# Kernel tuning notes

Hardware: AMD Instinct MI355X
Metric: run time of the kernel (lower is better)

The kernel has to match this reference:

```python
import jax, jax.numpy as jnp
import numpy as np

B, T, D, H = 2, 2048, 768, 12
DH = D // H  # 64

def setup_inputs() -> dict:
    key = jax.random.key(0)
    k1, k2, k3 = jax.random.split(key, 3)
    x = jax.random.normal(k1, (B, T, D), dtype=jnp.float32)
    W_qkv = jax.random.normal(k2, (D, 3 * D), dtype=jnp.float32) * (D ** -0.5)
    b_qkv = jax.random.normal(k3, (3 * D,), dtype=jnp.float32) * 0.02
    return {"x": x, "W_qkv": W_qkv, "b_qkv": b_qkv}

def reference(x, W_qkv, b_qkv):
    b, t, d = x.shape
    qkv = x @ W_qkv + b_qkv  # [b, t, 3*d]
    # 'b t (qkv h d) -> qkv b h t d'
    qkv = qkv.reshape(b, t, 3, H, DH).transpose(2, 0, 3, 1, 4)
    q, k, v = qkv[0], qkv[1], qkv[2]  # each [b, h, t, dh]
    scale = DH ** -0.5
    scores = jnp.einsum('bhid,bhjd->bhij', q, k) * scale  # [b, h, t, t]
    attn = jax.nn.softmax(scores, axis=-1)
    out = jnp.einsum('bhij,bhjd->bhid', attn, v)  # [b, h, t, dh]
    # 'b h t d -> b t (h d)'
    return out.transpose(0, 2, 1, 3).reshape(b, t, d)
```

## Files before the change

### kernel.cpp

```cpp
#include <hip/hip_runtime.h>
#include <hip/hip_bf16.h>
#include <stdint.h>

typedef __bf16 bf16_t;
typedef __bf16 v8bf  __attribute__((ext_vector_type(8)));
typedef __bf16 v4bf  __attribute__((ext_vector_type(4)));
typedef float  f32x4 __attribute__((ext_vector_type(4)));
typedef unsigned short u16x8 __attribute__((ext_vector_type(8)));

#define B_   2
#define T_   2048
#define D_   768
#define H_   12
#define DH_  64
#define N3_  2304
#define M_   4096
#define SPLIT_ 2

__device__ __forceinline__ void gll16(const void* g, void* l) {
  __builtin_amdgcn_global_load_lds(
      (const __attribute__((address_space(1))) void*)g,
      (__attribute__((address_space(3))) void*)l,
      16, 0, 0);
}

__device__ __forceinline__ float bf2f(unsigned short u) {
  union { unsigned u; float f; } x; x.u = ((unsigned)u) << 16; return x.f;
}

__global__ __launch_bounds__(256) void k_conv_x(const float* __restrict__ x,
                                                bf16_t* __restrict__ xb, int n4) {
  int i = blockIdx.x * 256 + threadIdx.x;
  if (i < n4) {
    float4 v = ((const float4*)x)[i];
    v4bf o = {(bf16_t)v.x, (bf16_t)v.y, (bf16_t)v.z, (bf16_t)v.w};
    *(v4bf*)(xb + (size_t)i * 4) = o;
  }
}

__global__ __launch_bounds__(256) void k_conv_wt(const float* __restrict__ W,
                                                 bf16_t* __restrict__ Wt) {
  __shared__ bf16_t tile[64 * 64];
  const int tid = threadIdx.x;
  const int n0 = blockIdx.x * 64;
  const int k0 = blockIdx.y * 64;
  #pragma unroll
  for (int rr = 0; rr < 4; ++rr) {
    int k  = rr * 16 + (tid >> 4);
    int gr = tid & 15;
    float4 v = *(const float4*)(W + (size_t)(k0 + k) * N3_ + n0 + gr * 4);
    v4bf o = {(bf16_t)v.x, (bf16_t)v.y, (bf16_t)v.z, (bf16_t)v.w};
    *(v4bf*)(tile + k * 64 + ((gr ^ (k & 15)) << 2)) = o;
  }
  __syncthreads();
  const int n = tid & 63, q = tid >> 6;
  bf16_t outv[16] __attribute__((aligned(16)));
  #pragma unroll
  for (int tt = 0; tt < 16; ++tt) {
    int k = q * 16 + tt;
    outv[tt] = tile[k * 64 + (((n >> 2) ^ (k & 15)) << 2) + (n & 3)];
  }
  bf16_t* dst = Wt + (size_t)(n0 + n) * D_ + k0 + q * 16;
  *(u16x8*)dst       = *(const u16x8*)outv;
  *((u16x8*)dst + 1) = *(const u16x8*)(outv + 8);
}

#define BK 32
__global__ __launch_bounds__(256) void k_gemm(const bf16_t* __restrict__ A,
                                              const bf16_t* __restrict__ Bt,
                                              const float*  __restrict__ bias,
                                              bf16_t* __restrict__ Cq,
                                              bf16_t* __restrict__ vt) {
  __shared__ bf16_t As[128 * BK];
  __shared__ bf16_t Bs[128 * BK];
  const int tid  = threadIdx.x;
  const int wave = tid >> 6, lane = tid & 63;
  const int g = lane >> 4, c = lane & 15;
  const int wy = wave >> 1, wx = wave & 1;
  const int bm = blockIdx.y * 128, bn = blockIdx.x * 128;

  const f32x4 zf = {0.f, 0.f, 0.f, 0.f};
  f32x4 acc[4][4];
  #pragma unroll
  for (int i = 0; i < 4; ++i)
    #pragma unroll
    for (int j = 0; j < 4; ++j) acc[i][j] = zf;

  const int rA = tid >> 2;
  const int kc = (tid & 3) * 8;

  for (int k0 = 0; k0 < D_; k0 += BK) {
    __syncthreads();
    #pragma unroll
    for (int cc = 0; cc < 2; ++cc) {
      gll16(A  + (size_t)(bm + cc * 64 + rA) * D_ + k0 + kc,
            (char*)As + cc * 4096 + wave * 1024);
      gll16(Bt + (size_t)(bn + cc * 64 + rA) * D_ + k0 + kc,
            (char*)Bs + cc * 4096 + wave * 1024);
    }
    __syncthreads();
    v8bf af[4], bfr[4];
    #pragma unroll
    for (int mi = 0; mi < 4; ++mi)
      af[mi] = *(const v8bf*)(As + (wy * 64 + mi * 16 + c) * BK + g * 8);
    #pragma unroll
    for (int ni = 0; ni < 4; ++ni)
      bfr[ni] = *(const v8bf*)(Bs + (wx * 64 + ni * 16 + c) * BK + g * 8);
    #pragma unroll
    for (int mi = 0; mi < 4; ++mi)
      #pragma unroll
      for (int ni = 0; ni < 4; ++ni)
        acc[mi][ni] = __builtin_amdgcn_mfma_f32_16x16x32_bf16(af[mi], bfr[ni], acc[mi][ni], 0, 0, 0);
  }

  if (bn >= 2 * D_) {
    const int hb = ((bn - 2 * D_) >> 6) + wx;
    #pragma unroll
    for (int ni = 0; ni < 4; ++ni) {
      float bv = bias[bn + wx * 64 + ni * 16 + c];
      const int d = ni * 16 + c;
      #pragma unroll
      for (int mi = 0; mi < 4; ++mi) {
        int row = bm + wy * 64 + mi * 16 + g * 4;
        int b = row >> 11, t = row & (T_ - 1);
        int tl = t & 63;
        int sp = (t & ~63) | (tl & 35) | ((tl & 12) << 1) | ((tl & 16) >> 2);
        v4bf o = {(bf16_t)(acc[mi][ni][0] + bv), (bf16_t)(acc[mi][ni][1] + bv),
                  (bf16_t)(acc[mi][ni][2] + bv), (bf16_t)(acc[mi][ni][3] + bv)};
        *(v4bf*)(vt + ((size_t)((b * H_ + hb) * DH_ + d)) * T_ + sp) = o;
      }
    }
  } else {
    const float qscale = (bn < D_) ? 0.18033688011112042f : 1.0f;
    #pragma unroll
    for (int ni = 0; ni < 4; ++ni) {
      float bv = bias[bn + wx * 64 + ni * 16 + c];
      #pragma unroll
      for (int mi = 0; mi < 4; ++mi) {
        int row = bm + wy * 64 + mi * 16 + g * 4;
        bf16_t* d0 = Cq + (size_t)row * N3_ + bn + wx * 64 + ni * 16 + c;
        #pragma unroll
        for (int j = 0; j < 4; ++j)
          d0[(size_t)j * N3_] = (bf16_t)((acc[mi][ni][j] + bv) * qscale);
      }
    }
  }
}

template<int SPLIT>
__global__ __launch_bounds__(256) void k_attn(const bf16_t* __restrict__ qkv,
                                              const bf16_t* __restrict__ vt,
                                              float* __restrict__ outp,
                                              float* __restrict__ lpart) {
  __shared__ __align__(16) bf16_t Ks[2][64 * 64];
  __shared__ __align__(16) bf16_t Vs[2][64 * 64];
  const int tid  = threadIdx.x;
  const int wave = tid >> 6, lane = tid & 63;
  const int g = lane >> 4, c = lane & 15;
  const int qt = blockIdx.x;
  const int bh = blockIdx.y;
  const int z  = (SPLIT > 1) ? blockIdx.z : 0;
  const int b = bh / H_, h = bh - b * H_;
  const int r0 = z * (T_ / SPLIT);

  v8bf aq[2];
  {
    const bf16_t* qb = qkv + ((size_t)(b * T_ + qt * 64 + wave * 16 + c)) * N3_ + h * DH_ + g * 8;
    aq[0] = *(const v8bf*)qb;
    aq[1] = *(const v8bf*)(qb + 32);
  }
  float lsum = 0.f;
  const f32x4 zf = {0.f, 0.f, 0.f, 0.f};
  f32x4 oacc[4];
  #pragma unroll
  for (int ni = 0; ni < 4; ++ni) oacc[ni] = zf;

  const int rS  = tid >> 3;
  const int grS = tid & 7;
  const bf16_t* gK[2];
  const bf16_t* gV[2];
  #pragma unroll
  for (int cc = 0; cc < 2; ++cc) {
    int r    = cc * 32 + rS;
    int colk = ((grS ^ (r & 7)) << 3);
    gK[cc] = qkv + ((size_t)(b * T_ + r0 + r)) * N3_ + D_ + h * DH_ + colk;
    gV[cc] = vt + ((size_t)(bh * DH_ + r)) * T_ + r0 + colk;
  }

  #pragma unroll
  for (int cc = 0; cc < 2; ++cc) {
    gll16(gK[cc], (char*)Ks[0] + cc * 4096 + wave * 1024);
    gll16(gV[cc], (char*)Vs[0] + cc * 4096 + wave * 1024);
    gK[cc] += 64 * (size_t)N3_;
    gV[cc] += 64;
  }
  __syncthreads();

#define ATTN_BODY(CUR, NXT, DOSTAGE)                                          \
  {                                                                           \
    if (DOSTAGE) {                                                            \
      _Pragma("unroll")                                                       \
      for (int cc = 0; cc < 2; ++cc) {                                        \
        gll16(gK[cc], (char*)Ks[NXT] + cc * 4096 + wave * 1024);              \
        gll16(gV[cc], (char*)Vs[NXT] + cc * 4096 + wave * 1024);              \
        gK[cc] += 64 * (size_t)N3_;                                           \
        gV[cc] += 64;                                                         \
      }                                                                       \
    }                                                                         \
    f32x4 s[4] = {zf, zf, zf, zf};                                            \
    __builtin_amdgcn_s_setprio(1);                                            \
    _Pragma("unroll")                                                         \
    for (int kk = 0; kk < 2; ++kk) {                                          \
      _Pragma("unroll")                                                       \
      for (int ni = 0; ni < 4; ++ni) {                                        \
        const int row = ni * 16 + c;                                          \
        v8bf bk = *(const v8bf*)(Ks[CUR] + row * 64 +                         \
                                 ((kk * 32 + g * 8) ^ ((row & 7) << 3)));     \
        s[ni] = __builtin_amdgcn_mfma_f32_16x16x32_bf16(bk, aq[kk], s[ni], 0, 0, 0); \
      }                                                                       \
    }                                                                         \
    __builtin_amdgcn_s_setprio(0);                                            \
    float rsub = 0.f;                                                         \
    v8bf apk[2];                                                              \
    _Pragma("unroll")                                                         \
    for (int ni = 0; ni < 4; ++ni) {                                          \
      float p0 = __builtin_amdgcn_exp2f(s[ni][0]);                            \
      float p1 = __builtin_amdgcn_exp2f(s[ni][1]);                            \
      float p2 = __builtin_amdgcn_exp2f(s[ni][2]);                            \
      float p3 = __builtin_amdgcn_exp2f(s[ni][3]);                            \
      rsub += (p0 + p1) + (p2 + p3);                                          \
      const int kkh = ni >> 1, off = (ni & 1) * 4;                            \
      apk[kkh][off + 0] = (bf16_t)p0;                                         \
      apk[kkh][off + 1] = (bf16_t)p1;                                         \
      apk[kkh][off + 2] = (bf16_t)p2;                                         \
      apk[kkh][off + 3] = (bf16_t)p3;                                         \
    }                                                                         \
    lsum += rsub;                                                             \
    __builtin_amdgcn_s_setprio(1);                                            \
    _Pragma("unroll")                                                         \
    for (int kk = 0; kk < 2; ++kk) {                                          \
      _Pragma("unroll")                                                       \
      for (int ni = 0; ni < 4; ++ni) {                                        \
        const int row = ni * 16 + c;                                          \
        v8bf bv = *(const v8bf*)(Vs[CUR] + row * 64 +                         \
                                 ((kk * 32 + g * 8) ^ ((row & 7) << 3)));     \
        oacc[ni] = __builtin_amdgcn_mfma_f32_16x16x32_bf16(bv, apk[kk], oacc[ni], 0, 0, 0); \
      }                                                                       \
    }                                                                         \
    __builtin_amdgcn_s_setprio(0);                                            \
    __syncthreads();                                                          \
  }

  const int NT2 = T_ / (64 * SPLIT * 2);
  for (int kt2 = 0; kt2 < NT2; ++kt2) {
    ATTN_BODY(0, 1, true)
    ATTN_BODY(1, 0, (kt2 < NT2 - 1))
  }
#undef ATTN_BODY

  lsum += __shfl_xor(lsum, 16);
  lsum += __shfl_xor(lsum, 32);
  const float inv = 1.0f / lsum;
  const int q = qt * 64 + wave * 16 + c;
  if (SPLIT > 1) {
    if (g == 0) lpart[(size_t)z * (B_ * H_ * T_) + (b * H_ + h) * T_ + q] = lsum;
    bf16_t* ob = (bf16_t*)outp + ((size_t)z * M_ * D_ + ((size_t)(b * T_ + q)) * D_ + h * DH_);
    #pragma unroll
    for (int ni = 0; ni < 4; ++ni) {
      v4bf o4 = {(bf16_t)(oacc[ni][0] * inv), (bf16_t)(oacc[ni][1] * inv),
                 (bf16_t)(oacc[ni][2] * inv), (bf16_t)(oacc[ni][3] * inv)};
      *(v4bf*)(ob + ni * 16 + g * 4) = o4;
    }
  } else {
    float* ob = outp + ((size_t)(b * T_ + q)) * D_ + h * DH_;
    #pragma unroll
    for (int ni = 0; ni < 4; ++ni) {
      float4 o4 = {oacc[ni][0] * inv, oacc[ni][1] * inv, oacc[ni][2] * inv, oacc[ni][3] * inv};
      *(float4*)(ob + ni * 16 + g * 4) = o4;
    }
  }
}

__global__ __launch_bounds__(256) void k_combine(const bf16_t* __restrict__ op,
                                                 const float* __restrict__ lp,
                                                 float* __restrict__ out) {
  const int i = blockIdx.x * 256 + threadIdx.x;
  const int e  = i * 8;
  const int tg = e / D_;
  const int d  = e - tg * D_;
  const int h  = d >> 6;
  const int b  = tg >> 11;
  const int t  = tg & (T_ - 1);
  const int li = (b * H_ + h) * T_ + t;
  float acc[8] = {0.f, 0.f, 0.f, 0.f, 0.f, 0.f, 0.f, 0.f};
  float ltot = 0.f;
  #pragma unroll
  for (int z = 0; z < SPLIT_; ++z) {
    const float lz = lp[(size_t)z * (B_ * H_ * T_) + li];
    ltot += lz;
    u16x8 u = *(const u16x8*)(op + (size_t)z * M_ * D_ + e);
    #pragma unroll
    for (int j = 0; j < 8; ++j) acc[j] += bf2f(u[j]) * lz;
  }
  const float inv = 1.0f / ltot;
  float4 o0 = {acc[0] * inv, acc[1] * inv, acc[2] * inv, acc[3] * inv};
  float4 o1 = {acc[4] * inv, acc[5] * inv, acc[6] * inv, acc[7] * inv};
  *(float4*)(out + e)     = o0;
  *(float4*)(out + e + 4) = o1;
}

extern "C" void kernel_launch(void* const* d_in, const int* in_sizes, int n_in,
                              void* d_out, int out_size, void* d_ws, size_t ws_size,
                              hipStream_t stream) {
  const float* x    = (const float*)d_in[0];
  const float* W    = (const float*)d_in[1];
  const float* bias = (const float*)d_in[2];
  float* out = (float*)d_out;
  char* ws = (char*)d_ws;
  bf16_t* xb    = (bf16_t*)(ws);
  bf16_t* wt    = (bf16_t*)(ws + 6291456);
  bf16_t* qkvb  = (bf16_t*)(ws + 9830400);
  bf16_t* vtb   = (bf16_t*)(ws + 28704768);
  bf16_t* opart = (bf16_t*)(ws + 34996224);
  float*  lpart = (float*)(ws + 47579136);
  const size_t need_split = 47972352;

  k_conv_x <<<dim3(3072),    dim3(256), 0, stream>>>(x, xb, (M_ * D_) / 4);
  k_conv_wt<<<dim3(36, 12),  dim3(256), 0, stream>>>(W, wt);
  k_gemm   <<<dim3(18, 32),  dim3(256), 0, stream>>>(xb, wt, bias, qkvb, vtb);
  if (ws_size >= need_split) {
    k_attn<SPLIT_><<<dim3(32, 24, SPLIT_), dim3(256), 0, stream>>>(qkvb, vtb, (float*)opart, lpart);
    k_combine<<<dim3(1536), dim3(256), 0, stream>>>(opart, lpart, out);
  } else {
    k_attn<1><<<dim3(32, 24), dim3(256), 0, stream>>>(qkvb, vtb, out, nullptr);
  }
}
```

Measured before the change: 83.18 us.

## Switch attention to 32x32x16 MFMA with two-wave blocks

The attention kernel moves from 16x16x32 MFMA tiles with 4 waves of 16 queries to 32x32x16 MFMA tiles with 2 waves of 32 queries each, giving 128-thread blocks. The V-transpose permutation in the GEMM epilogue is changed to match the new register layout of the probability operand. K/V staging is redistributed across the smaller block. The intent is fewer MFMA issues and less LDS operand traffic per FLOP, at the cost of larger accumulators, more register pressure, and fewer waves per block to hide latency.

```diff
diff --git a/kernel.cpp b/kernel.cpp
--- a/kernel.cpp
+++ b/kernel.cpp
@@ -6,6 +6,7 @@
 typedef __bf16 v8bf  __attribute__((ext_vector_type(8)));
 typedef __bf16 v4bf  __attribute__((ext_vector_type(4)));
 typedef float  f32x4 __attribute__((ext_vector_type(4)));
+typedef float  f32x16 __attribute__((ext_vector_type(16)));
 typedef unsigned short u16x8 __attribute__((ext_vector_type(8)));
 
 #define B_   2
@@ -124,7 +125,7 @@
         int row = bm + wy * 64 + mi * 16 + g * 4;
         int b = row >> 11, t = row & (T_ - 1);
         int tl = t & 63;
-        int sp = (t & ~63) | (tl & 35) | ((tl & 12) << 1) | ((tl & 16) >> 2);
+        int sp = (t & ~63) | (tl & 51) | ((tl & 4) << 1) | ((tl & 8) >> 1);
         v4bf o = {(bf16_t)(acc[mi][ni][0] + bv), (bf16_t)(acc[mi][ni][1] + bv),
                   (bf16_t)(acc[mi][ni][2] + bv), (bf16_t)(acc[mi][ni][3] + bv)};
         *(v4bf*)(vt + ((size_t)((b * H_ + hb) * DH_ + d)) * T_ + sp) = o;
@@ -148,7 +149,7 @@
 }
 
 template<int SPLIT>
-__global__ __launch_bounds__(256) void k_attn(const bf16_t* __restrict__ qkv,
+__global__ __launch_bounds__(128) void k_attn(const bf16_t* __restrict__ qkv,
                                               const bf16_t* __restrict__ vt,
                                               float* __restrict__ outp,
                                               float* __restrict__ lpart) {
@@ -156,96 +157,99 @@
   __shared__ __align__(16) bf16_t Vs[2][64 * 64];
   const int tid  = threadIdx.x;
   const int wave = tid >> 6, lane = tid & 63;
-  const int g = lane >> 4, c = lane & 15;
+  const int hi = lane >> 5, ql = lane & 31;
   const int qt = blockIdx.x;
   const int bh = blockIdx.y;
   const int z  = (SPLIT > 1) ? blockIdx.z : 0;
   const int b = bh / H_, h = bh - b * H_;
   const int r0 = z * (T_ / SPLIT);
-
-  v8bf aq[2];
+  const int q0 = qt * 64 + wave * 32;
+  const int swz = (ql & 7) << 3;
+
+  v8bf aq[4];
   {
-    const bf16_t* qb = qkv + ((size_t)(b * T_ + qt * 64 + wave * 16 + c)) * N3_ + h * DH_ + g * 8;
-    aq[0] = *(const v8bf*)qb;
-    aq[1] = *(const v8bf*)(qb + 32);
+    const bf16_t* qb = qkv + ((size_t)(b * T_ + q0 + ql)) * N3_ + h * DH_ + hi * 8;
+    #pragma unroll
+    for (int ds = 0; ds < 4; ++ds) aq[ds] = *(const v8bf*)(qb + ds * 16);
   }
   float lsum = 0.f;
-  const f32x4 zf = {0.f, 0.f, 0.f, 0.f};
-  f32x4 oacc[4];
-  #pragma unroll
-  for (int ni = 0; ni < 4; ++ni) oacc[ni] = zf;
+  f32x16 oacc0 = {0,0,0,0,0,0,0,0,0,0,0,0,0,0,0,0};
+  f32x16 oacc1 = {0,0,0,0,0,0,0,0,0,0,0,0,0,0,0,0};
 
   const int rS  = tid >> 3;
   const int grS = tid & 7;
-  const bf16_t* gK[2];
-  const bf16_t* gV[2];
-  #pragma unroll
-  for (int cc = 0; cc < 2; ++cc) {
-    int r    = cc * 32 + rS;
+  const bf16_t* gK[4];
+  const bf16_t* gV[4];
+  #pragma unroll
+  for (int cc = 0; cc < 4; ++cc) {
+    int r    = cc * 16 + rS;
     int colk = ((grS ^ (r & 7)) << 3);
     gK[cc] = qkv + ((size_t)(b * T_ + r0 + r)) * N3_ + D_ + h * DH_ + colk;
     gV[cc] = vt + ((size_t)(bh * DH_ + r)) * T_ + r0 + colk;
   }
 
   #pragma unroll
-  for (int cc = 0; cc < 2; ++cc) {
-    gll16(gK[cc], (char*)Ks[0] + cc * 4096 + wave * 1024);
-    gll16(gV[cc], (char*)Vs[0] + cc * 4096 + wave * 1024);
+  for (int cc = 0; cc < 4; ++cc) {
+    gll16(gK[cc], (char*)Ks[0] + cc * 2048 + wave * 1024);
+    gll16(gV[cc], (char*)Vs[0] + cc * 2048 + wave * 1024);
     gK[cc] += 64 * (size_t)N3_;
     gV[cc] += 64;
   }
   __syncthreads();
+
+#define PACK_APK(SV, KSB)                                                     \
+  _Pragma("unroll")                                                           \
+  for (int kq = 0; kq < 2; ++kq) {                                            \
+    v8bf tp;                                                                  \
+    _Pragma("unroll")                                                         \
+    for (int j = 0; j < 4; ++j) {                                             \
+      float pa = __builtin_amdgcn_exp2f(SV[(2 * kq) * 4 + j]);                \
+      float pb = __builtin_amdgcn_exp2f(SV[(2 * kq + 1) * 4 + j]);            \
+      rsub += pa + pb;                                                        \
+      tp[j] = (bf16_t)pa; tp[4 + j] = (bf16_t)pb;                             \
+    }                                                                         \
+    apk[(KSB) + kq] = tp;                                                     \
+  }
 
 #define ATTN_BODY(CUR, NXT, DOSTAGE)                                          \
   {                                                                           \
     if (DOSTAGE) {                                                            \
       _Pragma("unroll")                                                       \
-      for (int cc = 0; cc < 2; ++cc) {                                        \
-        gll16(gK[cc], (char*)Ks[NXT] + cc * 4096 + wave * 1024);              \
-        gll16(gV[cc], (char*)Vs[NXT] + cc * 4096 + wave * 1024);              \
+      for (int cc = 0; cc < 4; ++cc) {                                        \
+        gll16(gK[cc], (char*)Ks[NXT] + cc * 2048 + wave * 1024);              \
+        gll16(gV[cc], (char*)Vs[NXT] + cc * 2048 + wave * 1024);              \
         gK[cc] += 64 * (size_t)N3_;                                           \
         gV[cc] += 64;                                                         \
       }                                                                       \
     }                                                                         \
-    f32x4 s[4] = {zf, zf, zf, zf};                                            \
+    \
+    f32x16 s0 = {0,0,0,0,0,0,0,0,0,0,0,0,0,0,0,0};                            \
+    f32x16 s1 = {0,0,0,0,0,0,0,0,0,0,0,0,0,0,0,0};                            \
     __builtin_amdgcn_s_setprio(1);                                            \
     _Pragma("unroll")                                                         \
-    for (int kk = 0; kk < 2; ++kk) {                                          \
-      _Pragma("unroll")                                                       \
-      for (int ni = 0; ni < 4; ++ni) {                                        \
-        const int row = ni * 16 + c;                                          \
-        v8bf bk = *(const v8bf*)(Ks[CUR] + row * 64 +                         \
-                                 ((kk * 32 + g * 8) ^ ((row & 7) << 3)));     \
-        s[ni] = __builtin_amdgcn_mfma_f32_16x16x32_bf16(bk, aq[kk], s[ni], 0, 0, 0); \
-      }                                                                       \
+    for (int ds = 0; ds < 4; ++ds) {                                          \
+      const int colb = ds * 16 + hi * 8;                                      \
+      v8bf k0 = *(const v8bf*)(Ks[CUR] + ql * 64 + (colb ^ swz));             \
+      v8bf k1 = *(const v8bf*)(Ks[CUR] + (32 + ql) * 64 + (colb ^ swz));      \
+      s0 = __builtin_amdgcn_mfma_f32_32x32x16_bf16(k0, aq[ds], s0, 0, 0, 0);  \
+      s1 = __builtin_amdgcn_mfma_f32_32x32x16_bf16(k1, aq[ds], s1, 0, 0, 0);  \
     }                                                                         \
     __builtin_amdgcn_s_setprio(0);                                            \
+    \
+    v8bf apk[4];                                                              \
     float rsub = 0.f;                                                         \
-    v8bf apk[2];                                                              \
-    _Pragma("unroll")                                                         \
-    for (int ni = 0; ni < 4; ++ni) {                                          \
-      float p0 = __builtin_amdgcn_exp2f(s[ni][0]);                            \
-      float p1 = __builtin_amdgcn_exp2f(s[ni][1]);                            \
-      float p2 = __builtin_amdgcn_exp2f(s[ni][2]);                            \
-      float p3 = __builtin_amdgcn_exp2f(s[ni][3]);                            \
-      rsub += (p0 + p1) + (p2 + p3);                                          \
-      const int kkh = ni >> 1, off = (ni & 1) * 4;                            \
-      apk[kkh][off + 0] = (bf16_t)p0;                                         \
-      apk[kkh][off + 1] = (bf16_t)p1;                                         \
-      apk[kkh][off + 2] = (bf16_t)p2;                                         \
-      apk[kkh][off + 3] = (bf16_t)p3;                                         \
-    }                                                                         \
+    PACK_APK(s0, 0)                                                           \
+    PACK_APK(s1, 2)                                                           \
     lsum += rsub;                                                             \
+                                \
     __builtin_amdgcn_s_setprio(1);                                            \
     _Pragma("unroll")                                                         \
-    for (int kk = 0; kk < 2; ++kk) {                                          \
-      _Pragma("unroll")                                                       \
-      for (int ni = 0; ni < 4; ++ni) {                                        \
-        const int row = ni * 16 + c;                                          \
-        v8bf bv = *(const v8bf*)(Vs[CUR] + row * 64 +                         \
-                                 ((kk * 32 + g * 8) ^ ((row & 7) << 3)));     \
-        oacc[ni] = __builtin_amdgcn_mfma_f32_16x16x32_bf16(bv, apk[kk], oacc[ni], 0, 0, 0); \
-      }                                                                       \
+    for (int ks = 0; ks < 4; ++ks) {                                          \
+      const int colb = ks * 16 + hi * 8;                                      \
+      v8bf v0 = *(const v8bf*)(Vs[CUR] + ql * 64 + (colb ^ swz));             \
+      v8bf v1 = *(const v8bf*)(Vs[CUR] + (32 + ql) * 64 + (colb ^ swz));      \
+      oacc0 = __builtin_amdgcn_mfma_f32_32x32x16_bf16(v0, apk[ks], oacc0, 0, 0, 0); \
+      oacc1 = __builtin_amdgcn_mfma_f32_32x32x16_bf16(v1, apk[ks], oacc1, 0, 0, 0); \
     }                                                                         \
     __builtin_amdgcn_s_setprio(0);                                            \
     __syncthreads();                                                          \
@@ -257,26 +261,37 @@
     ATTN_BODY(1, 0, (kt2 < NT2 - 1))
   }
 #undef ATTN_BODY
-
-  lsum += __shfl_xor(lsum, 16);
+#undef PACK_APK
+
   lsum += __shfl_xor(lsum, 32);
   const float inv = 1.0f / lsum;
-  const int q = qt * 64 + wave * 16 + c;
+  const int q = q0 + ql;
   if (SPLIT > 1) {
-    if (g == 0) lpart[(size_t)z * (B_ * H_ * T_) + (b * H_ + h) * T_ + q] = lsum;
+    if (hi == 0) lpart[(size_t)z * (B_ * H_ * T_) + (b * H_ + h) * T_ + q] = lsum;
     bf16_t* ob = (bf16_t*)outp + ((size_t)z * M_ * D_ + ((size_t)(b * T_ + q)) * D_ + h * DH_);
     #pragma unroll
-    for (int ni = 0; ni < 4; ++ni) {
-      v4bf o4 = {(bf16_t)(oacc[ni][0] * inv), (bf16_t)(oacc[ni][1] * inv),
-                 (bf16_t)(oacc[ni][2] * inv), (bf16_t)(oacc[ni][3] * inv)};
-      *(v4bf*)(ob + ni * 16 + g * 4) = o4;
+    for (int db = 0; db < 2; ++db) {
+      const f32x16& oa = db ? oacc1 : oacc0;
+      #pragma unroll
+      for (int q4 = 0; q4 < 4; ++q4) {
+        const int d = db * 32 + q4 * 8 + hi * 4;
+        v4bf o4 = {(bf16_t)(oa[q4 * 4 + 0] * inv), (bf16_t)(oa[q4 * 4 + 1] * inv),
+                   (bf16_t)(oa[q4 * 4 + 2] * inv), (bf16_t)(oa[q4 * 4 + 3] * inv)};
+        *(v4bf*)(ob + d) = o4;
+      }
     }
   } else {
     float* ob = outp + ((size_t)(b * T_ + q)) * D_ + h * DH_;
     #pragma unroll
-    for (int ni = 0; ni < 4; ++ni) {
-      float4 o4 = {oacc[ni][0] * inv, oacc[ni][1] * inv, oacc[ni][2] * inv, oacc[ni][3] * inv};
-      *(float4*)(ob + ni * 16 + g * 4) = o4;
+    for (int db = 0; db < 2; ++db) {
+      const f32x16& oa = db ? oacc1 : oacc0;
+      #pragma unroll
+      for (int q4 = 0; q4 < 4; ++q4) {
+        const int d = db * 32 + q4 * 8 + hi * 4;
+        float4 o4 = {oa[q4 * 4 + 0] * inv, oa[q4 * 4 + 1] * inv,
+                     oa[q4 * 4 + 2] * inv, oa[q4 * 4 + 3] * inv};
+        *(float4*)(ob + d) = o4;
+      }
     }
   }
 }
@@ -329,9 +344,9 @@
   k_conv_wt<<<dim3(36, 12),  dim3(256), 0, stream>>>(W, wt);
   k_gemm   <<<dim3(18, 32),  dim3(256), 0, stream>>>(xb, wt, bias, qkvb, vtb);
   if (ws_size >= need_split) {
-    k_attn<SPLIT_><<<dim3(32, 24, SPLIT_), dim3(256), 0, stream>>>(qkvb, vtb, (float*)opart, lpart);
+    k_attn<SPLIT_><<<dim3(32, 24, SPLIT_), dim3(128), 0, stream>>>(qkvb, vtb, (float*)opart, lpart);
     k_combine<<<dim3(1536), dim3(256), 0, stream>>>(opart, lpart, out);
   } else {
-    k_attn<1><<<dim3(32, 24), dim3(256), 0, stream>>>(qkvb, vtb, out, nullptr);
-  }
-}
+    k_attn<1><<<dim3(32, 24), dim3(128), 0, stream>>>(qkvb, vtb, out, nullptr);
+  }
+}
```

Result: slower. 93.03 us (+11.8%).
